# Performance work log

Measured on AMD Instinct MI355X. Metric: run time of the kernel, lower is better.

## Reference

```python
import jax, jax.numpy as jnp
import numpy as np


def setup_inputs() -> dict:
    key = jax.random.key(0)
    B, C, D, H, W = 8, 2, 128, 96, 128
    corr = jax.random.normal(key, (B, C, D, H, W), dtype=jnp.float32)
    return {"corr": corr, "maxdisp": 50, "is_ux": 1}


def reference(corr, maxdisp, is_ux):
    # corr: (B, C, D, H, W). For each pixel (i, j) and displacement dx in
    # [-maxdisp, maxdisp], linearly interpolate corr along the D axis at
    # position (j + dx) if is_ux else (i + dx), with zero padding outside
    # [0, D-1] (matches grid_sample bilinear, align_corners=True, H==1).
    B, C, D, H, W = corr.shape
    K = 2 * maxdisp + 1
    dx = jnp.linspace(-float(maxdisp), float(maxdisp), K)  # (K,)
    if is_ux:
        base = jnp.broadcast_to(jnp.arange(W, dtype=jnp.float32)[None, :], (H, W))
    else:
        base = jnp.broadcast_to(jnp.arange(H, dtype=jnp.float32)[:, None], (H, W))
    pos = base[None, :, :] + dx[:, None, None]           # (K, H, W)
    i0f = jnp.floor(pos)
    w1 = (pos - i0f).astype(corr.dtype)                  # lerp weight for upper tap
    i0 = i0f.astype(jnp.int32)
    i1 = i0 + 1
    m0 = ((i0 >= 0) & (i0 < D)).astype(corr.dtype)       # zero-padding masks
    m1 = ((i1 >= 0) & (i1 < D)).astype(corr.dtype)
    idx0 = jnp.clip(i0, 0, D - 1)[None, None]            # (1,1,K,H,W) -> broadcast
    idx1 = jnp.clip(i1, 0, D - 1)[None, None]
    g0 = jnp.take_along_axis(corr, idx0, axis=2)         # (B, C, K, H, W)
    g1 = jnp.take_along_axis(corr, idx1, axis=2)
    out = g0 * ((1.0 - w1) * m0)[None, None] + g1 * (w1 * m1)[None, None]
    return out  # (B, C, 2*maxdisp+1, H, W)
```

## Files before the change

kernel.cpp:

```cpp
#include <hip/hip_runtime.h>


#define B_ 8
#define C_ 2
#define D_ 128
#define H_ 96
#define W_ 128
#define WT 64
#define KC 32
#define NKT 4
#define NT 512
#define RS 68
#define MAXR 96

__global__ __launch_bounds__(NT, 8) void corr2cost_kernel(
    const float* __restrict__ corr,
    const int* __restrict__ mp,
    const int* __restrict__ up,
    float* __restrict__ out) {
  __shared__ float lds[MAXR * RS];

  const int cpx = gridDim.x >> 3;
  const int raw = blockIdx.x;
  const int bid = (raw & 7) * cpx + (raw >> 3);

  const int kt    = bid & (NKT - 1);
  const int whalf = (bid >> 2) & 1;
  const int sl    = bid >> 3;
  const int h     = sl % H_;
  const int bc    = sl / H_;

  const int t  = threadIdx.x;
  const int m  = *mp;
  const int ux = *up;
  const int K  = 2 * m + 1;
  const int HW = H_ * W_;
  const int w0 = whalf * WT;
  const int k0 = kt * KC;

  const int bmin = ux ? w0 : h;
  const int bmax = ux ? (w0 + WT - 1) : h;
  const int khi  = (k0 + KC - 1 < K - 1) ? (k0 + KC - 1) : (K - 1);
  const int dlo  = bmin + k0 - m;
  const int dhi  = bmax + khi - m;
  const int dlo_c = dlo > 0 ? dlo : 0;
  const int dhi_c = dhi < D_ - 1 ? dhi : D_ - 1;
  const int R = dhi_c - dlo_c + 1;

  const float* __restrict__ src =
      corr + (size_t)bc * D_ * HW + (size_t)h * W_ + w0;
  const int nf4 = R * (WT / 4);
  for (int i = t; i < nf4; i += NT) {
    const int r  = i >> 4;
    const int w4 = (i & 15) * 4;
    const float4 v =
        *reinterpret_cast<const float4*>(src + (size_t)(dlo_c + r) * HW + w4);
    *reinterpret_cast<float4*>(&lds[r * RS + w4]) = v;
  }
  __syncthreads();

  const int wi   = t & (WT - 1);
  const int kg   = t >> 6;
  const int base = ux ? (w0 + wi) : h;
  float* __restrict__ dst =
      out + (size_t)bc * K * HW + (size_t)h * W_ + w0 + wi;

#pragma unroll
  for (int j = 0; j < KC / 8; ++j) {
    const int k = k0 + kg + j * 8;
    const int d = base + k - m;
    const bool ok = (unsigned)d < (unsigned)D_;
    int ld = d - dlo_c;
    ld = ld < 0 ? 0 : (ld > MAXR - 1 ? MAXR - 1 : ld);
    const float val = ok ? lds[ld * RS + wi] : 0.0f;
    if (k < K) dst[(size_t)k * HW] = val;
  }
}

extern "C" void kernel_launch(void* const* d_in, const int* in_sizes, int n_in,
                              void* d_out, int out_size, void* d_ws, size_t ws_size,
                              hipStream_t stream) {
  const float* corr    = (const float*)d_in[0];
  const int*   maxdisp = (const int*)d_in[1];
  const int*   is_ux   = (const int*)d_in[2];
  float*       out     = (float*)d_out;

  const int grid = B_ * C_ * H_ * 2 * NKT;
  corr2cost_kernel<<<grid, NT, 0, stream>>>(corr, maxdisp, is_ux, out);
}
```

Measured before the change: 180.2 us.

## Process all displacements per block instead of splitting K across four blocks

Each block now covers every displacement for its (b,c,h,half-row) slice, so the corr rows are staged into LDS once per slice rather than once per displacement chunk. The grid shrinks fourfold and the XCD-aware block remapping and LDS row padding are removed. Stores are batched seven at a time after the LDS reads. The trade-off is less parallelism (3072 blocks), a larger LDS footprint per block, and possible bank conflicts without the padding.

```diff
diff --git a/kernel.cpp b/kernel.cpp
--- a/kernel.cpp
+++ b/kernel.cpp
@@ -7,73 +7,69 @@
 #define H_ 96
 #define W_ 128
 #define WT 64
-#define KC 32
-#define NKT 4
 #define NT 512
-#define RS 68
-#define MAXR 96
+#define MAXR 114
 
-__global__ __launch_bounds__(NT, 8) void corr2cost_kernel(
+__global__ __launch_bounds__(NT) void corr2cost_kernel(
     const float* __restrict__ corr,
     const int* __restrict__ mp,
     const int* __restrict__ up,
     float* __restrict__ out) {
-  __shared__ float lds[MAXR * RS];
+  __shared__ float lds[MAXR * WT];
 
-  const int cpx = gridDim.x >> 3;
-  const int raw = blockIdx.x;
-  const int bid = (raw & 7) * cpx + (raw >> 3);
-
-  const int kt    = bid & (NKT - 1);
-  const int whalf = (bid >> 2) & 1;
-  const int sl    = bid >> 3;
+  const int t     = threadIdx.x;
+  const int bid   = blockIdx.x;
+  const int whalf = bid & 1;
+  const int sl    = bid >> 1;
   const int h     = sl % H_;
   const int bc    = sl / H_;
 
-  const int t  = threadIdx.x;
   const int m  = *mp;
   const int ux = *up;
   const int K  = 2 * m + 1;
   const int HW = H_ * W_;
   const int w0 = whalf * WT;
-  const int k0 = kt * KC;
 
   const int bmin = ux ? w0 : h;
   const int bmax = ux ? (w0 + WT - 1) : h;
-  const int khi  = (k0 + KC - 1 < K - 1) ? (k0 + KC - 1) : (K - 1);
-  const int dlo  = bmin + k0 - m;
-  const int dhi  = bmax + khi - m;
-  const int dlo_c = dlo > 0 ? dlo : 0;
-  const int dhi_c = dhi < D_ - 1 ? dhi : D_ - 1;
-  const int R = dhi_c - dlo_c + 1;
+  int dlo = bmin - m;        if (dlo < 0) dlo = 0;
+  int dhi = bmax + K - 1 - m; if (dhi > D_ - 1) dhi = D_ - 1;
+  const int R = dhi - dlo + 1;
 
   const float* __restrict__ src =
       corr + (size_t)bc * D_ * HW + (size_t)h * W_ + w0;
   const int nf4 = R * (WT / 4);
   for (int i = t; i < nf4; i += NT) {
     const int r  = i >> 4;
-    const int w4 = (i & 15) * 4;
-    const float4 v =
-        *reinterpret_cast<const float4*>(src + (size_t)(dlo_c + r) * HW + w4);
-    *reinterpret_cast<float4*>(&lds[r * RS + w4]) = v;
+    const int c4 = (i & 15) * 4;
+    *reinterpret_cast<float4*>(&lds[r * WT + c4]) =
+        *reinterpret_cast<const float4*>(src + (size_t)(dlo + r) * HW + c4);
   }
   __syncthreads();
 
-  const int wi   = t & (WT - 1);
-  const int kg   = t >> 6;
-  const int base = ux ? (w0 + wi) : h;
+  const int w    = t & (WT - 1);
+  const int kseg = t >> 6;
+  const int base = ux ? (w0 + w) : h;
   float* __restrict__ dst =
-      out + (size_t)bc * K * HW + (size_t)h * W_ + w0 + wi;
+      out + (size_t)bc * K * HW + (size_t)h * W_ + w0 + w;
 
+  const int NB = (K + 7) >> 3;
+  for (int kb = 0; kb < NB; kb += 7) {
+    float v[7];
 #pragma unroll
-  for (int j = 0; j < KC / 8; ++j) {
-    const int k = k0 + kg + j * 8;
-    const int d = base + k - m;
-    const bool ok = (unsigned)d < (unsigned)D_;
-    int ld = d - dlo_c;
-    ld = ld < 0 ? 0 : (ld > MAXR - 1 ? MAXR - 1 : ld);
-    const float val = ok ? lds[ld * RS + wi] : 0.0f;
-    if (k < K) dst[(size_t)k * HW] = val;
+    for (int j = 0; j < 7; ++j) {
+      const int k  = kseg + (kb + j) * 8;
+      const int d  = base + k - m;
+      const bool ok = (unsigned)d < (unsigned)D_;
+      int rr = d - dlo;
+      rr = rr < 0 ? 0 : (rr > MAXR - 1 ? MAXR - 1 : rr);
+      v[j] = ok ? lds[rr * WT + w] : 0.0f;
+    }
+#pragma unroll
+    for (int j = 0; j < 7; ++j) {
+      const int k = kseg + (kb + j) * 8;
+      if (k < K) dst[(size_t)k * HW] = v[j];
+    }
   }
 }
 
@@ -85,6 +81,6 @@
   const int*   is_ux   = (const int*)d_in[2];
   float*       out     = (float*)d_out;
 
-  const int grid = B_ * C_ * H_ * 2 * NKT;
+  const int grid = B_ * C_ * H_ * 2;
   corr2cost_kernel<<<grid, NT, 0, stream>>>(corr, maxdisp, is_ux, out);
 }
```

After: 173.0 us. 1.04x faster.
